# Optimization experiments

Measured on AMD Instinct MI355X. Metric: run time of the kernel, lower is better.

## Reference

```python
import jax, jax.numpy as jnp
import numpy as np

LNF, PNF, H = 128, 128, 128
THRESH = 10.0
NORM = 100.0
EPS = 1e-8


def _linear(x, W, b):
    return x @ W + b


def _glorot(key, shape):
    fan_in = shape[0]
    return jax.random.normal(key, shape, dtype=jnp.float32) / jnp.sqrt(jnp.float32(fan_in))


def setup_inputs() -> dict:
    key = jax.random.key(0)
    ks = jax.random.split(key, 20)
    bs, nl, npr = 4, 128, 1024
    inp = {
        "h_ligand": jax.random.normal(ks[0], (bs, nl, LNF), jnp.float32),
        "x_ligand": jax.random.normal(ks[1], (bs, nl, 3), jnp.float32) * 4.0,
        "h_protein": jax.random.normal(ks[2], (bs, npr, PNF), jnp.float32),
        "x_protein": jax.random.normal(ks[3], (bs, npr, 3), jnp.float32) * 4.0,
        "ligand_mask": jnp.ones((bs, nl, 1), jnp.float32),
        "protein_mask": jnp.ones((bs, npr, 1), jnp.float32),
        # attention MLP: (lnf+pnf+1)->H->H->1
        "aW1": _glorot(ks[4], (LNF + PNF + 1, H)), "ab1": jnp.zeros((H,), jnp.float32),
        "aW2": _glorot(ks[5], (H, H)),            "ab2": jnp.zeros((H,), jnp.float32),
        "aW3": _glorot(ks[6], (H, 1)),            "ab3": jnp.zeros((1,), jnp.float32),
        # value MLP: (pnf+1)->H->lnf
        "vW1": _glorot(ks[7], (PNF + 1, H)),      "vb1": jnp.zeros((H,), jnp.float32),
        "vW2": _glorot(ks[8], (H, LNF)),          "vb2": jnp.zeros((LNF,), jnp.float32),
        # coord MLP: (lnf+pnf+1)->H->1
        "cW1": _glorot(ks[9], (LNF + PNF + 1, H)), "cb1": jnp.zeros((H,), jnp.float32),
        "cW2": _glorot(ks[10], (H, 1)),           "cb2": jnp.zeros((1,), jnp.float32),
    }
    return inp


def reference(h_ligand, x_ligand, h_protein, x_protein, ligand_mask, protein_mask,
              aW1, ab1, aW2, ab2, aW3, ab3, vW1, vb1, vW2, vb2, cW1, cb1, cW2, cb2):
    bs, nl, lnf = h_ligand.shape
    npr = h_protein.shape[1]
    # pairwise geometry [bs, nl, np, ...]
    rel = x_ligand[:, :, None, :] - x_protein[:, None, :, :]
    ds = jnp.sum(rel * rel, axis=-1, keepdims=True)           # dist^2
    dist = jnp.sqrt(ds + EPS)
    edge = (dist < THRESH).astype(h_ligand.dtype)             # radius edge mask
    direction = rel / (dist + EPS)
    hl = jnp.broadcast_to(h_ligand[:, :, None, :], (bs, nl, npr, lnf))
    hp = jnp.broadcast_to(h_protein[:, None, :, :], (bs, nl, npr, h_protein.shape[-1]))
    pm = protein_mask[:, None, :, :]                          # [bs,1,np,1]

    pair_in = jnp.concatenate([hl, hp, ds], axis=-1)
    # attention MLP -> sigmoid
    a = jax.nn.silu(_linear(pair_in, aW1, ab1))
    a = jax.nn.silu(_linear(a, aW2, ab2))
    attn = jax.nn.sigmoid(_linear(a, aW3, ab3)) * pm
    # value MLP
    v = jax.nn.silu(_linear(jnp.concatenate([hp, ds], axis=-1), vW1, vb1))
    val = _linear(v, vW2, vb2)
    # feature messages, masked radius aggregation
    h_cross = jnp.sum(attn * val * edge, axis=2) / NORM       # [bs,nl,lnf]
    # coord MLP -> tanh
    c = jax.nn.silu(_linear(pair_in, cW1, cb1))
    cw = jnp.tanh(_linear(c, cW2, cb2)) * pm
    x_cross = jnp.sum(direction * cw * edge, axis=2) / NORM   # [bs,nl,3]

    h_cross = h_cross * ligand_mask
    x_cross = x_cross * ligand_mask
    return h_cross, x_cross
```

## Files before the change

kernel.cpp:

```cpp
#include <hip/hip_runtime.h>
#include <hip/hip_bf16.h>
#include <math.h>

#define HF 128
#define NL 128
#define NP 1024
#define NB 4
#define EPSF 1e-8f
#define NITEMS 2048

typedef short bf16x8 __attribute__((ext_vector_type(8)));
typedef float f32x4 __attribute__((ext_vector_type(4)));

__device__ __forceinline__ float fast_rcp(float x){ return __builtin_amdgcn_rcpf(x); }
__device__ __forceinline__ float silu_f(float x){ return x*fast_rcp(1.f+__expf(-x)); }
__device__ __forceinline__ float sigmoid_f(float x){ return fast_rcp(1.f+__expf(-x)); }
__device__ __forceinline__ float tanh_f(float x){ return 1.f - 2.f*fast_rcp(1.f+__expf(2.f*x)); }
__device__ __forceinline__ unsigned short f2bf(float f){ __hip_bfloat16 h=__float2bfloat16(f); return *(unsigned short*)&h; }
__device__ __forceinline__ float bf2f(short u){ unsigned int x = ((unsigned int)(unsigned short)u)<<16; float r; __builtin_memcpy(&r,&x,4); return r; }

__global__ __launch_bounds__(128) void precompute_kernel(
    const float* __restrict__ h_ligand, const float* __restrict__ h_protein,
    const float* __restrict__ aW1, const float* __restrict__ ab1,
    const float* __restrict__ vW1, const float* __restrict__ vb1,
    const float* __restrict__ cW1, const float* __restrict__ cb1,
    const float* __restrict__ aW2, const float* __restrict__ vW2,
    float* __restrict__ Al, float* __restrict__ Cl,
    unsigned short* __restrict__ Ap, unsigned short* __restrict__ Vp,
    unsigned short* __restrict__ Cp,
    unsigned short* __restrict__ WaT, unsigned short* __restrict__ WvT,
    int* __restrict__ counter)
{
    const int blk = blockIdx.x, n = threadIdx.x;
    if (blk < 64) {
        __shared__ float rows[8][HF];
        const int r0 = blk*8;
        for (int idx=n; idx<8*HF; idx+=128) rows[idx>>7][idx&127] = h_ligand[r0*HF+idx];
        __syncthreads();
        float aA[8], aC[8];
        const float bA = ab1[n], bC = cb1[n];
        #pragma unroll
        for (int r=0;r<8;++r){ aA[r]=bA; aC[r]=bC; }
        #pragma unroll 4
        for (int k=0;k<HF;++k){
            float wA = aW1[k*HF+n], wC = cW1[k*HF+n];
            #pragma unroll
            for (int r=0;r<8;++r){ aA[r]=fmaf(rows[r][k],wA,aA[r]); aC[r]=fmaf(rows[r][k],wC,aC[r]); }
        }
        #pragma unroll
        for (int r=0;r<8;++r){ Al[(r0+r)*HF+n]=aA[r]; Cl[(r0+r)*HF+n]=aC[r]; }
    } else if (blk < 1088) {
        __shared__ float rows[4][HF];
        const int r0 = (blk-64)*4;
        for (int idx=n; idx<4*HF; idx+=128) rows[idx>>7][idx&127] = h_protein[r0*HF+idx];
        __syncthreads();
        float aA[4], aV[4], aC[4];
        const float bV = vb1[n];
        #pragma unroll
        for (int r=0;r<4;++r){ aA[r]=0.f; aV[r]=bV; aC[r]=0.f; }
        #pragma unroll 2
        for (int k=0;k<HF;++k){
            float wA = aW1[(HF+k)*HF+n], wV = vW1[k*HF+n], wC = cW1[(HF+k)*HF+n];
            #pragma unroll
            for (int r=0;r<4;++r){
                float h = rows[r][k];
                aA[r]=fmaf(h,wA,aA[r]); aV[r]=fmaf(h,wV,aV[r]); aC[r]=fmaf(h,wC,aC[r]);
            }
        }
        #pragma unroll
        for (int r=0;r<4;++r){
            Ap[(r0+r)*HF+n]=f2bf(aA[r]); Vp[(r0+r)*HF+n]=f2bf(aV[r]); Cp[(r0+r)*HF+n]=f2bf(aC[r]);
        }
    } else {
        const int m = blk - 1088;
        if (m == 0 && n == 0) *counter = 0;
        const float* W = (m<8) ? aW2 : vW2;
        unsigned short* WT = (m<8) ? WaT : WvT;
        const int n0 = (m&7)*16;
        #pragma unroll
        for (int kb=0; kb<16; ++kb) {
            int k = kb*8 + (n>>4);
            int col = n0 + (n&15);
            WT[col*HF + k] = f2bf(W[k*HF + col]);
        }
    }
}

__global__ __launch_bounds__(256,2) void egnn_main_kernel(
    const float* __restrict__ x_ligand, const float* __restrict__ x_protein,
    const float* __restrict__ ligand_mask, const float* __restrict__ protein_mask,
    const float* __restrict__ aW1, const float* __restrict__ ab2,
    const float* __restrict__ aW3, const float* __restrict__ ab3,
    const float* __restrict__ vW1, const float* __restrict__ vb2,
    const float* __restrict__ cW1, const float* __restrict__ cW2, const float* __restrict__ cb2,
    const float* __restrict__ Al, const float* __restrict__ Cl,
    const unsigned short* __restrict__ Ap, const unsigned short* __restrict__ Vp,
    const unsigned short* __restrict__ Cp,
    const unsigned short* __restrict__ WaT, const unsigned short* __restrict__ WvT,
    int* __restrict__ counter,
    float* __restrict__ out)
{
    __shared__ __align__(16) char wt[32768];
    __shared__ float ds_all[256], pme[256], dirx[256], diry[256], dirz[256];
    __shared__ unsigned short jlist[256];
    __shared__ float Al_s[HF], Cl_s[HF];
    __shared__ float aw1l[HF], cw1l[HF], vw1l[HF], cW2s[HF];
    __shared__ float attn_part[64], attn_e[32];
    __shared__ float hred[256];
    __shared__ float xw[12];
    __shared__ int nact_s, cur_s;

    const int t = threadIdx.x, lane = t&63, w = t>>6;
    const int wj = w>>1, wn = w&1;
    const int lr = lane&15, lg = lane>>4;

    if (t < HF) {
        aw1l[t] = aW1[256*HF+t];
        cw1l[t] = cW1[256*HF+t];
        vw1l[t] = vW1[128*HF+t];
        cW2s[t] = cW2[t];
    }
    float ab2v[4], aw3v[4], vb2v[4];
    #pragma unroll
    for (int nt=0; nt<4; ++nt) {
        int n = wn*64 + nt*16 + lr;
        ab2v[nt] = ab2[n]; aw3v[nt] = aW3[n]; vb2v[nt] = vb2[n];
    }
    const float ab3v = ab3[0], cb2v = cb2[0];

    for (int c = t; c < 2048; c += 256) {
        int n = c >> 4, kc = c & 15;
        *(bf16x8*)(wt + n*256 + ((kc*16) ^ ((n&7)<<4))) = *(const bf16x8*)(WaT + n*HF + kc*8);
    }
    __syncthreads();
    bf16x8 wa[4][4], wv[4][4];
    #pragma unroll
    for (int nt = 0; nt < 4; ++nt) {
        int ncol = wn*64 + nt*16 + lr;
        int rb = ncol*256, sw = (ncol & 7) << 4;
        #pragma unroll
        for (int ks = 0; ks < 4; ++ks)
            wa[nt][ks] = *(bf16x8*)(wt + rb + ((lg*16 + ks*64) ^ sw));
    }
    __syncthreads();
    for (int c = t; c < 2048; c += 256) {
        int n = c >> 4, kc = c & 15;
        *(bf16x8*)(wt + n*256 + ((kc*16) ^ ((n&7)<<4))) = *(const bf16x8*)(WvT + n*HF + kc*8);
    }
    __syncthreads();
    #pragma unroll
    for (int nt = 0; nt < 4; ++nt) {
        int ncol = wn*64 + nt*16 + lr;
        int rb = ncol*256, sw = (ncol & 7) << 4;
        #pragma unroll
        for (int ks = 0; ks < 4; ++ks)
            wv[nt][ks] = *(bf16x8*)(wt + rb + ((lg*16 + ks*64) ^ sw));
    }

    const int brow = t >> 4, bcol = (t & 15)*8;
    const int crow = t >> 3, cg = t & 7;

    for (;;) {
        __syncthreads();
        if (t == 0) cur_s = atomicAdd(counter, 1);
        __syncthreads();
        const int item = cur_s;
        if (item >= NITEMS) break;
        const int ii = item >> 2;
        const int q  = item & 3;
        const int b  = ii >> 7;
        const int jbase = q*256;

        if (t < HF) {
            Al_s[t] = Al[(size_t)ii*HF+t];
            Cl_s[t] = Cl[(size_t)ii*HF+t];
        }
        const float xl0 = x_ligand[ii*3+0], xl1 = x_ligand[ii*3+1], xl2 = x_ligand[ii*3+2];
        const float* xp = x_protein + ((size_t)b*NP + jbase)*3;
        const float* pm = protein_mask + (size_t)b*NP + jbase;
        {
            const int jj = t;
            float r0 = xl0-xp[jj*3+0], r1 = xl1-xp[jj*3+1], r2 = xl2-xp[jj*3+2];
            float ds = r0*r0+r1*r1+r2*r2;
            float dist = sqrtf(ds+EPSF);
            float inv = fast_rcp(dist+EPSF);
            float e = dist < 10.f ? 1.f : 0.f;
            ds_all[jj]=ds; pme[jj]=pm[jj]*e;
            dirx[jj]=r0*inv; diry[jj]=r1*inv; dirz[jj]=r2*inv;
        }
        __syncthreads();
        if (w == 0) {
            int base = 0;
            #pragma unroll
            for (int c=0; c<4; ++c) {
                int jj = c*64 + lane;
                bool act = pme[jj] > 0.f;
                unsigned long long m = __ballot(act);
                int pos = base + __popcll(m & ((1ull<<lane)-1ull));
                if (act) jlist[pos] = (unsigned short)jj;
                base += __popcll(m);
            }
            if (lane == 0) nact_s = base;
        }
        __syncthreads();
        const int nact = nact_s;
        if (nact == 0) continue;
        const int ntiles = (nact + 31) >> 5;

        const unsigned short* Ap_b = Ap + ((size_t)b*NP + jbase)*HF;
        const unsigned short* Vp_b = Vp + ((size_t)b*NP + jbase)*HF;
        const unsigned short* Cp_b = Cp + ((size_t)b*NP + jbase)*HF;

        float hacc[4] = {0.f,0.f,0.f,0.f};
        float sae = 0.f;
        float xa0 = 0.f, xa1 = 0.f, xa2 = 0.f;

        for (int tile = 0; tile < ntiles; ++tile) {
            const int j0 = tile*32;

            #pragma unroll
            for (int m = 0; m < 2; ++m) {
                const int row = m*16 + brow;
                const int grow = j0 + row;
                const int jl = jlist[grow < nact ? grow : 0];
                const float dsv = ds_all[jl];
                bf16x8 ap = *(const bf16x8*)(Ap_b + (size_t)jl*HF + bcol);
                f32x4 al0 = *(const f32x4*)&Al_s[bcol];
                f32x4 al1 = *(const f32x4*)&Al_s[bcol+4];
                f32x4 w0  = *(const f32x4*)&aw1l[bcol];
                f32x4 w1  = *(const f32x4*)&aw1l[bcol+4];
                bf16x8 pk;
                #pragma unroll
                for (int qq = 0; qq < 4; ++qq) {
                    pk[qq]   = (short)f2bf(silu_f(al0[qq] + bf2f(ap[qq])   + dsv*w0[qq]));
                    pk[qq+4] = (short)f2bf(silu_f(al1[qq] + bf2f(ap[qq+4]) + dsv*w1[qq]));
                }
                *(bf16x8*)(wt + row*256 + ((bcol*2) ^ ((row & 7) << 4))) = pk;
            }
            __syncthreads();

            bf16x8 af[4];
            {
                int arow = wj*16 + lr;
                int rb = arow*256, sw = (arow & 7) << 4;
                #pragma unroll
                for (int ks = 0; ks < 4; ++ks)
                    af[ks] = *(bf16x8*)(wt + rb + ((lg*16 + ks*64) ^ sw));
            }
            f32x4 acc[4];
            #pragma unroll
            for (int nt = 0; nt < 4; ++nt) {
                acc[nt] = (f32x4){0.f,0.f,0.f,0.f};
                #pragma unroll
                for (int ks = 0; ks < 4; ++ks)
                    acc[nt] = __builtin_amdgcn_mfma_f32_16x16x32_bf16(af[ks], wa[nt][ks], acc[nt], 0,0,0);
            }
            {
                const int growc = j0 + crow;
                const bool okc = growc < nact;
                const int jlc = jlist[okc ? growc : 0];
                const float pmec = okc ? pme[jlc] : 0.f;
                const float dsc = ds_all[jlc];
                float part = 0.f;
                const unsigned short* cp = Cp_b + (size_t)jlc*HF + cg*16;
                #pragma unroll
                for (int u = 0; u < 2; ++u) {
                    const int ch = cg*16 + u*8;
                    bf16x8 cv = *(const bf16x8*)(cp + u*8);
                    f32x4 cl0 = *(const f32x4*)&Cl_s[ch];
                    f32x4 cl1 = *(const f32x4*)&Cl_s[ch+4];
                    f32x4 w0  = *(const f32x4*)&cw1l[ch];
                    f32x4 w1  = *(const f32x4*)&cw1l[ch+4];
                    f32x4 s0  = *(const f32x4*)&cW2s[ch];
                    f32x4 s1  = *(const f32x4*)&cW2s[ch+4];
                    #pragma unroll
                    for (int qq = 0; qq < 4; ++qq) {
                        part += silu_f(cl0[qq] + bf2f(cv[qq])   + dsc*w0[qq]) * s0[qq];
                        part += silu_f(cl1[qq] + bf2f(cv[qq+4]) + dsc*w1[qq]) * s1[qq];
                    }
                }
                part += __shfl_xor(part,1); part += __shfl_xor(part,2); part += __shfl_xor(part,4);
                if (cg == 0) {
                    float cw = tanh_f(part + cb2v) * pmec;
                    xa0 = fmaf(dirx[jlc], cw, xa0);
                    xa1 = fmaf(diry[jlc], cw, xa1);
                    xa2 = fmaf(dirz[jlc], cw, xa2);
                }
            }
            #pragma unroll
            for (int r = 0; r < 4; ++r) {
                float p = 0.f;
                #pragma unroll
                for (int nt = 0; nt < 4; ++nt)
                    p += silu_f(acc[nt][r] + ab2v[nt]) * aw3v[nt];
                p += __shfl_xor(p,1); p += __shfl_xor(p,2);
                p += __shfl_xor(p,4); p += __shfl_xor(p,8);
                if (lr == 0) attn_part[wn*32 + wj*16 + lg*4 + r] = p;
            }
            __syncthreads();

            if (t < 32) {
                const int grow = j0 + t;
                const bool ok = grow < nact;
                const int j = jlist[ok ? grow : 0];
                attn_e[t] = sigmoid_f(attn_part[t] + attn_part[32+t] + ab3v) * (ok ? pme[j] : 0.f);
            }
            #pragma unroll
            for (int m = 0; m < 2; ++m) {
                const int row = m*16 + brow;
                const int grow = j0 + row;
                const int jl = jlist[grow < nact ? grow : 0];
                const float dsv = ds_all[jl];
                bf16x8 vp = *(const bf16x8*)(Vp_b + (size_t)jl*HF + bcol);
                f32x4 w0 = *(const f32x4*)&vw1l[bcol];
                f32x4 w1 = *(const f32x4*)&vw1l[bcol+4];
                bf16x8 pk;
                #pragma unroll
                for (int qq = 0; qq < 4; ++qq) {
                    pk[qq]   = (short)f2bf(silu_f(bf2f(vp[qq])   + dsv*w0[qq]));
                    pk[qq+4] = (short)f2bf(silu_f(bf2f(vp[qq+4]) + dsv*w1[qq]));
                }
                *(bf16x8*)(wt + 8192 + row*256 + ((bcol*2) ^ ((row & 7) << 4))) = pk;
            }
            __syncthreads();

            bf16x8 vf[4];
            {
                int arow = wj*16 + lr;
                int rb = 8192 + arow*256, sw = (arow & 7) << 4;
                #pragma unroll
                for (int ks = 0; ks < 4; ++ks)
                    vf[ks] = *(bf16x8*)(wt + rb + ((lg*16 + ks*64) ^ sw));
            }
            float ae[4];
            #pragma unroll
            for (int r = 0; r < 4; ++r) { ae[r] = attn_e[wj*16 + lg*4 + r]; sae += ae[r]; }
            #pragma unroll
            for (int nt = 0; nt < 4; ++nt) {
                f32x4 a = (f32x4){0.f,0.f,0.f,0.f};
                #pragma unroll
                for (int ks = 0; ks < 4; ++ks)
                    a = __builtin_amdgcn_mfma_f32_16x16x32_bf16(vf[ks], wv[nt][ks], a, 0,0,0);
                hacc[nt] += ae[0]*a[0] + ae[1]*a[1] + ae[2]*a[2] + ae[3]*a[3];
            }
        }

        #pragma unroll
        for (int nt = 0; nt < 4; ++nt) {
            hacc[nt] += __shfl_xor(hacc[nt],16);
            hacc[nt] += __shfl_xor(hacc[nt],32);
        }
        sae += __shfl_xor(sae,16);
        sae += __shfl_xor(sae,32);
        if (lg == 0) {
            #pragma unroll
            for (int nt = 0; nt < 4; ++nt)
                hred[wj*128 + wn*64 + nt*16 + lr] = hacc[nt] + vb2v[nt]*sae;
        }
        xa0 += __shfl_xor(xa0,1);  xa1 += __shfl_xor(xa1,1);  xa2 += __shfl_xor(xa2,1);
        xa0 += __shfl_xor(xa0,2);  xa1 += __shfl_xor(xa1,2);  xa2 += __shfl_xor(xa2,2);
        xa0 += __shfl_xor(xa0,4);  xa1 += __shfl_xor(xa1,4);  xa2 += __shfl_xor(xa2,4);
        xa0 += __shfl_xor(xa0,8);  xa1 += __shfl_xor(xa1,8);  xa2 += __shfl_xor(xa2,8);
        xa0 += __shfl_xor(xa0,16); xa1 += __shfl_xor(xa1,16); xa2 += __shfl_xor(xa2,16);
        xa0 += __shfl_xor(xa0,32); xa1 += __shfl_xor(xa1,32); xa2 += __shfl_xor(xa2,32);
        if (lane == 0) { xw[w*3+0]=xa0; xw[w*3+1]=xa1; xw[w*3+2]=xa2; }
        __syncthreads();

        const float lm = ligand_mask[ii];
        if (t < HF) {
            float v = (hred[t] + hred[128+t]) * 0.01f * lm;
            atomicAdd(&out[(size_t)ii*HF + t], v);
        }
        if (t < 3) {
            float v = (xw[t] + xw[3+t] + xw[6+t] + xw[9+t]) * 0.01f * lm;
            atomicAdd(&out[(size_t)NB*NL*HF + ii*3 + t], v);
        }
    }
}

extern "C" void kernel_launch(void* const* d_in, const int* in_sizes, int n_in,
                              void* d_out, int out_size, void* d_ws, size_t ws_size,
                              hipStream_t stream) {
    const float* h_ligand     = (const float*)d_in[0];
    const float* x_ligand     = (const float*)d_in[1];
    const float* h_protein    = (const float*)d_in[2];
    const float* x_protein    = (const float*)d_in[3];
    const float* ligand_mask  = (const float*)d_in[4];
    const float* protein_mask = (const float*)d_in[5];
    const float* aW1 = (const float*)d_in[6];
    const float* ab1 = (const float*)d_in[7];
    const float* aW2 = (const float*)d_in[8];
    const float* ab2 = (const float*)d_in[9];
    const float* aW3 = (const float*)d_in[10];
    const float* ab3 = (const float*)d_in[11];
    const float* vW1 = (const float*)d_in[12];
    const float* vb1 = (const float*)d_in[13];
    const float* vW2 = (const float*)d_in[14];
    const float* vb2 = (const float*)d_in[15];
    const float* cW1 = (const float*)d_in[16];
    const float* cb1 = (const float*)d_in[17];
    const float* cW2 = (const float*)d_in[18];
    const float* cb2 = (const float*)d_in[19];

    float* Al = (float*)d_ws;
    float* Cl = Al + 512*HF;
    unsigned short* Ap  = (unsigned short*)(Cl + 512*HF);
    unsigned short* Vp  = Ap + (size_t)NB*NP*HF;
    unsigned short* Cp  = Vp + (size_t)NB*NP*HF;
    unsigned short* WaT = Cp + (size_t)NB*NP*HF;
    unsigned short* WvT = WaT + HF*HF;
    int* counter        = (int*)(WvT + HF*HF);

    hipMemsetAsync(d_out, 0, (size_t)out_size*sizeof(float), stream);

    precompute_kernel<<<1104, 128, 0, stream>>>(
        h_ligand, h_protein, aW1, ab1, vW1, vb1, cW1, cb1, aW2, vW2,
        Al, Cl, Ap, Vp, Cp, WaT, WvT, counter);

    egnn_main_kernel<<<768, 256, 0, stream>>>(
        x_ligand, x_protein, ligand_mask, protein_mask,
        aW1, ab2, aW3, ab3, vW1, vb2, cW1, cW2, cb2,
        Al, Cl, Ap, Vp, Cp, WaT, WvT, counter, (float*)d_out);
}
```

Baseline: 259.2 us.

## Shrink LDS and register footprint, fuse output zeroing, raise persistent grid size

The weight staging buffer is halved by loading WaT/WvT in two 64-column halves, each consumed only by the matching warp half. Per-thread bias and output-weight arrays move from registers into shared memory, lowering register pressure. Together these aim to fit more resident blocks, so the persistent grid grows from 768 to 1024. The output memset is replaced by zeroing inside the precompute kernel, saving a launch; in exchange, the inner loop now does extra LDS reads.

```diff
diff --git a/kernel.cpp b/kernel.cpp
--- a/kernel.cpp
+++ b/kernel.cpp
@@ -8,6 +8,7 @@
 #define NB 4
 #define EPSF 1e-8f
 #define NITEMS 2048
+#define OUT_N (NB*NL*HF + NB*NL*3)
 
 typedef short bf16x8 __attribute__((ext_vector_type(8)));
 typedef float f32x4 __attribute__((ext_vector_type(4)));
@@ -29,9 +30,13 @@
     unsigned short* __restrict__ Ap, unsigned short* __restrict__ Vp,
     unsigned short* __restrict__ Cp,
     unsigned short* __restrict__ WaT, unsigned short* __restrict__ WvT,
-    int* __restrict__ counter)
+    int* __restrict__ counter, float* __restrict__ out)
 {
     const int blk = blockIdx.x, n = threadIdx.x;
+    {
+        int gid = blk*128 + n;
+        if (gid < OUT_N) out[gid] = 0.f;
+    }
     if (blk < 64) {
         __shared__ float rows[8][HF];
         const int r0 = blk*8;
@@ -100,11 +105,13 @@
     int* __restrict__ counter,
     float* __restrict__ out)
 {
-    __shared__ __align__(16) char wt[32768];
+    __shared__ __align__(16) char wt[16384];
     __shared__ float ds_all[256], pme[256], dirx[256], diry[256], dirz[256];
     __shared__ unsigned short jlist[256];
     __shared__ float Al_s[HF], Cl_s[HF];
     __shared__ float aw1l[HF], cw1l[HF], vw1l[HF], cW2s[HF];
+    __shared__ float2 aa3[HF];
+    __shared__ float vb2s[HF];
     __shared__ float attn_part[64], attn_e[32];
     __shared__ float hred[256];
     __shared__ float xw[12];
@@ -119,42 +126,51 @@
         cw1l[t] = cW1[256*HF+t];
         vw1l[t] = vW1[128*HF+t];
         cW2s[t] = cW2[t];
-    }
-    float ab2v[4], aw3v[4], vb2v[4];
-    #pragma unroll
-    for (int nt=0; nt<4; ++nt) {
-        int n = wn*64 + nt*16 + lr;
-        ab2v[nt] = ab2[n]; aw3v[nt] = aW3[n]; vb2v[nt] = vb2[n];
+        aa3[t]  = make_float2(ab2[t], aW3[t]);
+        vb2s[t] = vb2[t];
     }
     const float ab3v = ab3[0], cb2v = cb2[0];
 
-    for (int c = t; c < 2048; c += 256) {
-        int n = c >> 4, kc = c & 15;
-        *(bf16x8*)(wt + n*256 + ((kc*16) ^ ((n&7)<<4))) = *(const bf16x8*)(WaT + n*HF + kc*8);
-    }
-    __syncthreads();
     bf16x8 wa[4][4], wv[4][4];
     #pragma unroll
-    for (int nt = 0; nt < 4; ++nt) {
-        int ncol = wn*64 + nt*16 + lr;
-        int rb = ncol*256, sw = (ncol & 7) << 4;
-        #pragma unroll
-        for (int ks = 0; ks < 4; ++ks)
-            wa[nt][ks] = *(bf16x8*)(wt + rb + ((lg*16 + ks*64) ^ sw));
-    }
-    __syncthreads();
-    for (int c = t; c < 2048; c += 256) {
-        int n = c >> 4, kc = c & 15;
-        *(bf16x8*)(wt + n*256 + ((kc*16) ^ ((n&7)<<4))) = *(const bf16x8*)(WvT + n*HF + kc*8);
-    }
-    __syncthreads();
+    for (int h = 0; h < 2; ++h) {
+        __syncthreads();
+        for (int c = t; c < 1024; c += 256) {
+            int nloc = c >> 4, kc = c & 15;
+            *(bf16x8*)(wt + nloc*256 + ((kc*16) ^ ((nloc&7)<<4))) =
+                *(const bf16x8*)(WaT + (size_t)(h*64 + nloc)*HF + kc*8);
+        }
+        __syncthreads();
+        if (wn == h) {
+            #pragma unroll
+            for (int nt = 0; nt < 4; ++nt) {
+                int nloc = nt*16 + lr;
+                int rb = nloc*256, sw = (nloc & 7) << 4;
+                #pragma unroll
+                for (int ks = 0; ks < 4; ++ks)
+                    wa[nt][ks] = *(bf16x8*)(wt + rb + ((lg*16 + ks*64) ^ sw));
+            }
+        }
+    }
     #pragma unroll
-    for (int nt = 0; nt < 4; ++nt) {
-        int ncol = wn*64 + nt*16 + lr;
-        int rb = ncol*256, sw = (ncol & 7) << 4;
-        #pragma unroll
-        for (int ks = 0; ks < 4; ++ks)
-            wv[nt][ks] = *(bf16x8*)(wt + rb + ((lg*16 + ks*64) ^ sw));
+    for (int h = 0; h < 2; ++h) {
+        __syncthreads();
+        for (int c = t; c < 1024; c += 256) {
+            int nloc = c >> 4, kc = c & 15;
+            *(bf16x8*)(wt + nloc*256 + ((kc*16) ^ ((nloc&7)<<4))) =
+                *(const bf16x8*)(WvT + (size_t)(h*64 + nloc)*HF + kc*8);
+        }
+        __syncthreads();
+        if (wn == h) {
+            #pragma unroll
+            for (int nt = 0; nt < 4; ++nt) {
+                int nloc = nt*16 + lr;
+                int rb = nloc*256, sw = (nloc & 7) << 4;
+                #pragma unroll
+                for (int ks = 0; ks < 4; ++ks)
+                    wv[nt][ks] = *(bf16x8*)(wt + rb + ((lg*16 + ks*64) ^ sw));
+            }
+        }
     }
 
     const int brow = t >> 4, bcol = (t & 15)*8;
@@ -291,8 +307,10 @@
             for (int r = 0; r < 4; ++r) {
                 float p = 0.f;
                 #pragma unroll
-                for (int nt = 0; nt < 4; ++nt)
-                    p += silu_f(acc[nt][r] + ab2v[nt]) * aw3v[nt];
+                for (int nt = 0; nt < 4; ++nt) {
+                    float2 c2 = aa3[wn*64 + nt*16 + lr];
+                    p += silu_f(acc[nt][r] + c2.x) * c2.y;
+                }
                 p += __shfl_xor(p,1); p += __shfl_xor(p,2);
                 p += __shfl_xor(p,4); p += __shfl_xor(p,8);
                 if (lr == 0) attn_part[wn*32 + wj*16 + lg*4 + r] = p;
@@ -355,7 +373,7 @@
         if (lg == 0) {
             #pragma unroll
             for (int nt = 0; nt < 4; ++nt)
-                hred[wj*128 + wn*64 + nt*16 + lr] = hacc[nt] + vb2v[nt]*sae;
+                hred[wj*128 + wn*64 + nt*16 + lr] = hacc[nt] + vb2s[wn*64 + nt*16 + lr]*sae;
         }
         xa0 += __shfl_xor(xa0,1);  xa1 += __shfl_xor(xa1,1);  xa2 += __shfl_xor(xa2,1);
         xa0 += __shfl_xor(xa0,2);  xa1 += __shfl_xor(xa1,2);  xa2 += __shfl_xor(xa2,2);
@@ -411,13 +429,11 @@
     unsigned short* WvT = WaT + HF*HF;
     int* counter        = (int*)(WvT + HF*HF);
 
-    hipMemsetAsync(d_out, 0, (size_t)out_size*sizeof(float), stream);
-
     precompute_kernel<<<1104, 128, 0, stream>>>(
         h_ligand, h_protein, aW1, ab1, vW1, vb1, cW1, cb1, aW2, vW2,
-        Al, Cl, Ap, Vp, Cp, WaT, WvT, counter);
-
-    egnn_main_kernel<<<768, 256, 0, stream>>>(
+        Al, Cl, Ap, Vp, Cp, WaT, WvT, counter, (float*)d_out);
+
+    egnn_main_kernel<<<1024, 256, 0, stream>>>(
         x_ligand, x_protein, ligand_mask, protein_mask,
         aW1, ab2, aW3, ab3, vW1, vb2, cW1, cW2, cb2,
         Al, Cl, Ap, Vp, Cp, WaT, WvT, counter, (float*)d_out);
```

Result: no change. 255.6 us (-1.4%).
